# Optimization experiments

Measured on AMD Instinct MI355X. Metric: run time of the kernel, lower is better.

Reference implementation:

```python
import jax, jax.numpy as jnp
import numpy as np

S, B, H, T = 1024, 32, 1024, 512


def setup_inputs() -> dict:
    key = jax.random.key(0)
    ks = jax.random.split(key, 7)
    scale = 1.0 / np.sqrt(H)
    return {
        "hidden": jax.random.normal(ks[0], (S, B, H), dtype=jnp.float32),
        "x": jax.random.normal(ks[1], (B, T, H), dtype=jnp.float32),
        "problem_q": jax.random.normal(ks[2], (B, H), dtype=jnp.float32),
        "K_w": jax.random.normal(ks[3], (H, H), dtype=jnp.float32) * scale,
        "K_b": jax.random.normal(ks[4], (H,), dtype=jnp.float32) * scale,
        "V_w": jax.random.normal(ks[5], (H, H), dtype=jnp.float32) * scale,
        "V_b": jax.random.normal(ks[6], (H,), dtype=jnp.float32) * scale,
    }


def reference(hidden, x, problem_q, K_w, K_b, V_w, V_b):
    # hidden: [S, B, H] -> hidden2: [B, S, H]
    hidden2 = jnp.transpose(hidden, (1, 0, 2))
    # Linear projections (torch Linear: y = x @ W.T + b)
    k = jnp.einsum("bsh,kh->bsk", hidden2, K_w) + K_b  # [B, S, H]
    v = jnp.einsum("bsh,kh->bsk", hidden2, V_w) + V_b  # [B, S, H]
    # scores[b,t,s] = x[b,t] . k[b,s]  (QK^T per batch)
    scores = jnp.einsum("bth,bsh->bts", x, k)
    attn = jax.nn.softmax(scores, axis=-1)  # softmax over encoder positions S
    out = jax.nn.sigmoid(jnp.einsum("bts,bsh->bth", attn, v))  # [B, T, H]
    return out
```

## Files before the change

### kernel.cpp

```cpp
#include <hip/hip_runtime.h>

typedef unsigned short u16;
typedef __attribute__((ext_vector_type(8))) short short8;
typedef __attribute__((ext_vector_type(8))) _Float16 half8;
typedef __attribute__((ext_vector_type(4))) float f32x4;
typedef __attribute__((ext_vector_type(4))) u16 u16x4;
typedef __attribute__((ext_vector_type(4))) unsigned int u32x4;

#define DEVINL static __device__ __forceinline__

DEVINL u16 f2bf(float f) {
  unsigned u = __builtin_bit_cast(unsigned, f);
  u += 0x7fffu + ((u >> 16) & 1u);
  return (u16)(u >> 16);
}
DEVINL float bf2f(u16 h) {
  return __builtin_bit_cast(float, ((unsigned)h) << 16);
}
DEVINL u16 f2h(float f) { return __builtin_bit_cast(u16, (_Float16)f); }
DEVINL float h2f(u16 h) { return (float)__builtin_bit_cast(_Float16, h); }

DEVINL void gload16(const void* g, void* l) {
  __builtin_amdgcn_global_load_lds(
      (const __attribute__((address_space(1))) void*)g,
      (__attribute__((address_space(3))) void*)l, 16, 0, 0);
}

#define BAR() asm volatile("s_barrier" ::: "memory")
#define WAIT_VM0() asm volatile("s_waitcnt vmcnt(0)" ::: "memory")
#define WAIT_LGKM0() asm volatile("s_waitcnt lgkmcnt(0)" ::: "memory")


__global__ __launch_bounds__(256) void cvt_hidden2_k(const float* __restrict__ hid,
                                                     u16* __restrict__ hf,
                                                     u16* __restrict__ hT) {
  __shared__ u16 tl[64][72];
  const int s0 = blockIdx.x * 64;
  const int h0 = blockIdx.y * 64;
  const int b = blockIdx.z;
  const int t = threadIdx.x;
  const int r = t >> 4;
  const int c4 = (t & 15) * 4;
#pragma unroll
  for (int it = 0; it < 4; ++it) {
    const int s = it * 16 + r;
    const f32x4 v = *(const f32x4*)(hid + ((size_t)(s0 + s) * 32 + b) * 1024 + h0 + c4);
    u16x4 of;
#pragma unroll
    for (int j = 0; j < 4; ++j) {
      of[j] = f2h(v[j]);
      tl[s][c4 + j] = f2bf(v[j]);
    }
    *(u16x4*)(hf + ((size_t)b * 1024 + s0 + s) * 1024 + h0 + c4) = of;
  }
  __syncthreads();
  const int h = t >> 2;
  const int sq = (t & 3) * 16;
  u16 tmp[16] __attribute__((aligned(16)));
#pragma unroll
  for (int i = 0; i < 16; ++i) tmp[i] = tl[sq + i][h];
  u16* dst = hT + ((size_t)b * 1024 + h0 + h) * 1024 + s0 + sq;
  *(u32x4*)(dst) = *(const u32x4*)&tmp[0];
  *(u32x4*)(dst + 8) = *(const u32x4*)&tmp[8];
}

__global__ __launch_bounds__(256) void cvt_split_k(const float* __restrict__ in,
                                                   u16* __restrict__ hi_o,
                                                   u16* __restrict__ lo_o, long n4) {
  long i = (long)blockIdx.x * 256 + threadIdx.x;
  const long stride = (long)gridDim.x * 256;
  for (; i < n4; i += stride) {
    const f32x4 v = ((const f32x4*)in)[i];
    u16x4 oh, ol;
#pragma unroll
    for (int j = 0; j < 4; ++j) {
      const u16 hi = f2bf(v[j]);
      oh[j] = hi;
      ol[j] = f2bf(v[j] - bf2f(hi));
    }
    ((u16x4*)hi_o)[i] = oh;
    ((u16x4*)lo_o)[i] = ol;
  }
}

__global__ __launch_bounds__(256) void cvt_f32_bf16_k(const float* __restrict__ in,
                                                      u16* __restrict__ out, long n4) {
  long i = (long)blockIdx.x * 256 + threadIdx.x;
  const long stride = (long)gridDim.x * 256;
  for (; i < n4; i += stride) {
    const f32x4 v = ((const f32x4*)in)[i];
    u16x4 o;
#pragma unroll
    for (int j = 0; j < 4; ++j) o[j] = f2bf(v[j]);
    ((u16x4*)out)[i] = o;
  }
}

__global__ __launch_bounds__(256) void cvt_w_split_t_k(const float* __restrict__ in,
                                                       u16* __restrict__ hi_o,
                                                       u16* __restrict__ lo_o) {
  __shared__ float tile[64][65];
  const int bh = blockIdx.x * 64;
  const int bj = blockIdx.y * 64;
  const int t = threadIdx.x;
  const int r = t >> 4;
  const int c4 = (t & 15) * 4;
#pragma unroll
  for (int it = 0; it < 4; ++it) {
    const int row = it * 16 + r;
    const f32x4 v = *(const f32x4*)(in + (size_t)(bj + row) * 1024 + bh + c4);
#pragma unroll
    for (int j = 0; j < 4; ++j) tile[c4 + j][row] = v[j];
  }
  __syncthreads();
#pragma unroll
  for (int it = 0; it < 4; ++it) {
    const int hrow = it * 16 + r;
    u16x4 oh, ol;
#pragma unroll
    for (int j = 0; j < 4; ++j) {
      const float f = tile[hrow][c4 + j];
      const u16 hv = f2bf(f);
      oh[j] = hv;
      ol[j] = f2bf(f - bf2f(hv));
    }
    *(u16x4*)(hi_o + (size_t)(bh + hrow) * 1024 + bj + c4) = oh;
    *(u16x4*)(lo_o + (size_t)(bh + hrow) * 1024 + bj + c4) = ol;
  }
}

__global__ __launch_bounds__(512) void gemm3_8ph_k(
    const u16* __restrict__ Ah, const u16* __restrict__ Al,
    const u16* __restrict__ Bh, const u16* __restrict__ Bl,
    u16* __restrict__ Chi, u16* __restrict__ Clo) {
  __shared__ u16 lds[2][2][256 * 64];
  const int bid = blockIdx.x;
  const int swz = (bid & 7) * 32 + (bid >> 3);
  const int m0 = (swz >> 2) * 256;
  const int n0 = (swz & 3) * 256;
  const int tid = threadIdx.x;
  const int lane = tid & 63, wid = tid >> 6;
  const int wr = wid >> 2, wc = wid & 3;
  const int fr = lane & 15, fk = lane >> 4;

  f32x4 acc[8][4] = {};

#define STAGE3(pb, q, gph, gpl, rb, kt)                                        \
  {                                                                            \
    _Pragma("unroll") for (int j = 0; j < 4; ++j) {                            \
      const int slot = j * 512 + tid;                                          \
      const int r = slot >> 3;                                                 \
      const int g = (slot & 7) ^ (r & 7);                                      \
      const u16* src = (g < 4) ? (gph) : (gpl);                                \
      gload16(src + (size_t)((rb) + r) * 1024 + (kt) * 32 + (g & 3) * 8,       \
              &lds[pb][q][(j * 512 + wid * 64) * 8]);                          \
    }                                                                          \
  }

  STAGE3(0, 0, Ah, Al, m0, 0);
  STAGE3(0, 1, Bh, Bl, n0, 0);

  for (int t = 0; t < 32; ++t) {
    const int p = t & 1;
    WAIT_VM0();
    BAR();
    short8 bh[4], bl[4];
#pragma unroll
    for (int ph = 0; ph < 4; ++ph) {
      short8 ah[2], al[2];
#pragma unroll
      for (int i = 0; i < 2; ++i) {
        const int r = wr * 128 + (ph * 2 + i) * 16 + fr;
        const int ch = fk ^ (r & 7);
        ah[i] = *(const short8*)&lds[p][0][r * 64 + ch * 8];
        al[i] = *(const short8*)&lds[p][0][r * 64 + (ch ^ 4) * 8];
      }
      if (ph == 0) {
#pragma unroll
        for (int nf = 0; nf < 4; ++nf) {
          const int rn = wc * 64 + nf * 16 + fr;
          const int cn = fk ^ (rn & 7);
          bh[nf] = *(const short8*)&lds[p][1][rn * 64 + cn * 8];
          bl[nf] = *(const short8*)&lds[p][1][rn * 64 + (cn ^ 4) * 8];
        }
        if (t < 31) STAGE3(p ^ 1, 0, Ah, Al, m0, t + 1);
      }
      if (ph == 1 && t < 31) STAGE3(p ^ 1, 1, Bh, Bl, n0, t + 1);
      BAR();
      WAIT_LGKM0();
      __builtin_amdgcn_sched_barrier(0);
      __builtin_amdgcn_s_setprio(1);
#pragma unroll
      for (int i = 0; i < 2; ++i)
#pragma unroll
        for (int nf = 0; nf < 4; ++nf) {
          acc[ph * 2 + i][nf] =
              __builtin_amdgcn_mfma_f32_16x16x32_bf16(ah[i], bh[nf], acc[ph * 2 + i][nf], 0, 0, 0);
          acc[ph * 2 + i][nf] =
              __builtin_amdgcn_mfma_f32_16x16x32_bf16(ah[i], bl[nf], acc[ph * 2 + i][nf], 0, 0, 0);
          acc[ph * 2 + i][nf] =
              __builtin_amdgcn_mfma_f32_16x16x32_bf16(al[i], bh[nf], acc[ph * 2 + i][nf], 0, 0, 0);
        }
      __builtin_amdgcn_s_setprio(0);
      BAR();
    }
  }
#undef STAGE3

  const int cb = n0 + wc * 64 + fr;
  const int rb = m0 + wr * 128 + fk * 4;
#pragma unroll
  for (int mf = 0; mf < 8; ++mf)
#pragma unroll
    for (int nf = 0; nf < 4; ++nf) {
      const int col = cb + nf * 16;
#pragma unroll
      for (int j = 0; j < 4; ++j) {
        const int row = rb + mf * 16 + j;
        const float kv = acc[mf][nf][j];
        const u16 hi = f2h(kv);
        Chi[(size_t)row * 1024 + col] = hi;
        Clo[(size_t)row * 1024 + col] = f2h(kv - h2f(hi));
      }
    }
}

__global__ __launch_bounds__(512) void gemm2_8ph_k(
    const u16* __restrict__ Qh_, const u16* __restrict__ Ql_,
    const u16* __restrict__ Hf_, float* __restrict__ S) {
  __shared__ u16 lA[2][256 * 64];
  __shared__ u16 lB[2][256 * 32];
  const int bid = blockIdx.x;
  const int swz = (bid & 7) * 32 + (bid >> 3);
  const int z = swz >> 3;
  const int m0 = ((swz >> 2) & 1) * 256;
  const int n0 = (swz & 3) * 256;
  const u16* Qh = Qh_ + (size_t)z * 512 * 1024;
  const u16* Ql = Ql_ + (size_t)z * 512 * 1024;
  const u16* Hf = Hf_ + (size_t)z * 1024 * 1024;
  float* Cf = S + (size_t)z * 512 * 1024;
  const int tid = threadIdx.x;
  const int lane = tid & 63, wid = tid >> 6;
  const int wr = wid >> 2, wc = wid & 3;
  const int fr = lane & 15, fk = lane >> 4;

  f32x4 acc[8][4] = {};

#define STAGEA(pb, kt)                                                         \
  {                                                                            \
    _Pragma("unroll") for (int j = 0; j < 4; ++j) {                            \
      const int slot = j * 512 + tid;                                          \
      const int r = slot >> 3;                                                 \
      const int g = (slot & 7) ^ (r & 7);                                      \
      const u16* src = (g < 4) ? Qh : Ql;                                      \
      gload16(src + (size_t)(m0 + r) * 1024 + (kt) * 32 + (g & 3) * 8,         \
              &lA[pb][(j * 512 + wid * 64) * 8]);                              \
    }                                                                          \
  }
#define STAGEB(pb, kt)                                                         \
  {                                                                            \
    _Pragma("unroll") for (int j = 0; j < 2; ++j) {                            \
      const int slot = j * 512 + tid;                                          \
      const int r = slot >> 2;                                                 \
      const int g = (slot & 3) ^ ((r >> 1) & 3);                               \
      gload16(Hf + (size_t)(n0 + r) * 1024 + (kt) * 32 + g * 8,                \
              &lB[pb][(j * 512 + wid * 64) * 8]);                              \
    }                                                                          \
  }

  STAGEA(0, 0);
  STAGEB(0, 0);

  for (int t = 0; t < 32; ++t) {
    const int p = t & 1;
    WAIT_VM0();
    BAR();
    half8 bf[4];
#pragma unroll
    for (int ph = 0; ph < 4; ++ph) {
      half8 ah[2], al[2];
#pragma unroll
      for (int i = 0; i < 2; ++i) {
        const int r = wr * 128 + (ph * 2 + i) * 16 + fr;
        const int ch = fk ^ (r & 7);
        ah[i] = *(const half8*)&lA[p][r * 64 + ch * 8];
        al[i] = *(const half8*)&lA[p][r * 64 + (ch ^ 4) * 8];
      }
      if (ph == 0) {
#pragma unroll
        for (int nf = 0; nf < 4; ++nf) {
          const int rn = wc * 64 + nf * 16 + fr;
          const int cn = fk ^ ((rn >> 1) & 3);
          bf[nf] = *(const half8*)&lB[p][rn * 32 + cn * 8];
        }
        if (t < 31) STAGEA(p ^ 1, t + 1);
      }
      if (ph == 1 && t < 31) STAGEB(p ^ 1, t + 1);
      BAR();
      WAIT_LGKM0();
      __builtin_amdgcn_sched_barrier(0);
      __builtin_amdgcn_s_setprio(1);
#pragma unroll
      for (int i = 0; i < 2; ++i)
#pragma unroll
        for (int nf = 0; nf < 4; ++nf) {
          acc[ph * 2 + i][nf] =
              __builtin_amdgcn_mfma_f32_16x16x32_f16(ah[i], bf[nf], acc[ph * 2 + i][nf], 0, 0, 0);
          acc[ph * 2 + i][nf] =
              __builtin_amdgcn_mfma_f32_16x16x32_f16(al[i], bf[nf], acc[ph * 2 + i][nf], 0, 0, 0);
        }
      __builtin_amdgcn_s_setprio(0);
      BAR();
    }
  }
#undef STAGEA
#undef STAGEB

  const int cb = n0 + wc * 64 + fr;
  const int rb = m0 + wr * 128 + fk * 4;
#pragma unroll
  for (int mf = 0; mf < 8; ++mf)
#pragma unroll
    for (int nf = 0; nf < 4; ++nf) {
      const int col = cb + nf * 16;
#pragma unroll
      for (int j = 0; j < 4; ++j) {
        const int row = rb + mf * 16 + j;
        Cf[(size_t)row * 1024 + col] = acc[mf][nf][j];
      }
    }
}

template <int CM>
__global__ __launch_bounds__(512) void gemm1_8ph_k(
    const u16* __restrict__ A_, const u16* __restrict__ Bt_,
    const float* __restrict__ bias, void* __restrict__ Cout) {
  __shared__ u16 lds[2][2][256 * 64];
  const int bid = blockIdx.x;
  const int swz = (bid & 7) * 32 + (bid >> 3);
  int m0, n0;
  const u16 *A, *Bt;
  float* Cf = nullptr;
  u16* Cb = nullptr;
  if (CM == 0) {
    const int z = swz >> 3;
    m0 = ((swz >> 2) & 1) * 256;
    n0 = (swz & 3) * 256;
    A = A_ + (size_t)z * 512 * 1024;
    Bt = Bt_ + (size_t)z * 1024 * 1024;
    Cb = (u16*)Cout + (size_t)z * 512 * 1024;
  } else {
    m0 = (swz >> 2) * 256;
    n0 = (swz & 3) * 256;
    A = A_; Bt = Bt_;
    Cf = (float*)Cout;
  }
  const int tid = threadIdx.x;
  const int lane = tid & 63, wid = tid >> 6;
  const int wr = wid >> 2, wc = wid & 3;
  const int fr = lane & 15, fk = lane >> 4;

  f32x4 acc[8][4] = {};

#define STAGE1(pb, q, gp, rb, kt)                                              \
  {                                                                            \
    _Pragma("unroll") for (int j = 0; j < 4; ++j) {                            \
      const int slot = j * 512 + tid;                                          \
      const int r = slot >> 3;                                                 \
      const int g = (slot & 7) ^ (r & 7);                                      \
      gload16((gp) + (size_t)((rb) + r) * 1024 + (kt) * 64 + g * 8,            \
              &lds[pb][q][(j * 512 + wid * 64) * 8]);                          \
    }                                                                          \
  }

  STAGE1(0, 0, A, m0, 0);
  STAGE1(0, 1, Bt, n0, 0);

  for (int t = 0; t < 16; ++t) {
    const int p = t & 1;
    WAIT_VM0();
    BAR();
    short8 bfr[4][2];
#pragma unroll
    for (int ph = 0; ph < 4; ++ph) {
      short8 a[2][2];
#pragma unroll
      for (int i = 0; i < 2; ++i) {
        const int r = wr * 128 + (ph * 2 + i) * 16 + fr;
#pragma unroll
        for (int ks = 0; ks < 2; ++ks) {
          const int g = (ks * 4 + fk) ^ (r & 7);
          a[i][ks] = *(const short8*)&lds[p][0][r * 64 + g * 8];
        }
      }
      if (ph == 0) {
#pragma unroll
        for (int nf = 0; nf < 4; ++nf) {
          const int rn = wc * 64 + nf * 16 + fr;
#pragma unroll
          for (int ks = 0; ks < 2; ++ks) {
            const int g = (ks * 4 + fk) ^ (rn & 7);
            bfr[nf][ks] = *(const short8*)&lds[p][1][rn * 64 + g * 8];
          }
        }
        if (t < 15) {
          STAGE1(p ^ 1, 0, A, m0, t + 1);
          STAGE1(p ^ 1, 1, Bt, n0, t + 1);
        }
      }
      BAR();
      WAIT_LGKM0();
      __builtin_amdgcn_sched_barrier(0);
      __builtin_amdgcn_s_setprio(1);
#pragma unroll
      for (int i = 0; i < 2; ++i)
#pragma unroll
        for (int nf = 0; nf < 4; ++nf) {
          acc[ph * 2 + i][nf] = __builtin_amdgcn_mfma_f32_16x16x32_bf16(
              a[i][0], bfr[nf][0], acc[ph * 2 + i][nf], 0, 0, 0);
          acc[ph * 2 + i][nf] = __builtin_amdgcn_mfma_f32_16x16x32_bf16(
              a[i][1], bfr[nf][1], acc[ph * 2 + i][nf], 0, 0, 0);
        }
      __builtin_amdgcn_s_setprio(0);
      BAR();
    }
  }
#undef STAGE1

  const int cb = n0 + wc * 64 + fr;
  const int rb = m0 + wr * 128 + fk * 4;
  if (CM == 0) {
#pragma unroll
    for (int mf = 0; mf < 8; ++mf)
#pragma unroll
      for (int nf = 0; nf < 4; ++nf) {
        const int col = cb + nf * 16;
#pragma unroll
        for (int j = 0; j < 4; ++j) {
          const int row = rb + mf * 16 + j;
          Cb[(size_t)row * 1024 + col] = f2bf(acc[mf][nf][j]);
        }
      }
  } else {
#pragma unroll
    for (int mf = 0; mf < 8; ++mf)
#pragma unroll
      for (int nf = 0; nf < 4; ++nf) {
        const int col = cb + nf * 16;
        const float bv = bias[col];
#pragma unroll
        for (int j = 0; j < 4; ++j) {
          const int row = rb + mf * 16 + j;
          const float xv = acc[mf][nf][j] + bv;
          Cf[(size_t)row * 1024 + col] = 1.0f / (1.0f + __expf(-xv));
        }
      }
  }
}

__global__ __launch_bounds__(256) void softmax_k(const float* __restrict__ S,
                                                 u16* __restrict__ Attn) {
  const float* rp = S + (size_t)blockIdx.x * 1024;
  const int tid = threadIdx.x;
  const int lane = tid & 63, wid = tid >> 6;
  const f32x4 v = ((const f32x4*)rp)[tid];
  float mx = fmaxf(fmaxf(v[0], v[1]), fmaxf(v[2], v[3]));
#pragma unroll
  for (int off = 32; off; off >>= 1) mx = fmaxf(mx, __shfl_xor(mx, off));
  __shared__ float red[4];
  __shared__ float red2[4];
  if (lane == 0) red[wid] = mx;
  __syncthreads();
  mx = fmaxf(fmaxf(red[0], red[1]), fmaxf(red[2], red[3]));
  const float e0 = __expf(v[0] - mx), e1 = __expf(v[1] - mx);
  const float e2 = __expf(v[2] - mx), e3 = __expf(v[3] - mx);
  float s = (e0 + e1) + (e2 + e3);
#pragma unroll
  for (int off = 32; off; off >>= 1) s += __shfl_xor(s, off);
  if (lane == 0) red2[wid] = s;
  __syncthreads();
  const float inv = 1.0f / (red2[0] + red2[1] + red2[2] + red2[3]);
  u16x4 o;
  o[0] = f2bf(e0 * inv); o[1] = f2bf(e1 * inv); o[2] = f2bf(e2 * inv); o[3] = f2bf(e3 * inv);
  ((u16x4*)(Attn + (size_t)blockIdx.x * 1024))[tid] = o;
}

extern "C" void kernel_launch(void* const* d_in, const int* in_sizes, int n_in,
                              void* d_out, int out_size, void* d_ws, size_t ws_size,
                              hipStream_t stream) {
  const float* hidden = (const float*)d_in[0];
  const float* x = (const float*)d_in[1];
  const float* K_w = (const float*)d_in[3];
  const float* V_w = (const float*)d_in[5];
  const float* V_b = (const float*)d_in[6];

  char* ws = (char*)d_ws;
  u16* hf16 = (u16*)(ws);
  u16* hT = (u16*)(ws + 67108864);
  u16* qhi = (u16*)(ws + 134217728);
  u16* qlo = (u16*)(ws + 167772160);
  float* scoresF = (float*)(ws + 201326592);
  u16* attn = hf16;
  u16* ctx = qhi;
  u16* kwt_h = (u16*)(ws + 268435456);
  u16* kwt_l = kwt_h + 1024 * 1024;
  u16* vw = kwt_h + 2 * 1024 * 1024;
  u16* xhi = (u16*)d_out;
  u16* xlo = xhi + 32L * 512 * 1024;
  float* out = (float*)d_out;

  cvt_hidden2_k<<<dim3(16, 16, 32), 256, 0, stream>>>(hidden, hf16, hT);
  cvt_split_k<<<2048, 256, 0, stream>>>(x, xhi, xlo, 32L * 512 * 1024 / 4);
  cvt_w_split_t_k<<<dim3(16, 16), 256, 0, stream>>>(K_w, kwt_h, kwt_l);
  cvt_f32_bf16_k<<<1024, 256, 0, stream>>>(V_w, vw, 1024L * 1024 / 4);
  gemm3_8ph_k<<<256, 512, 0, stream>>>(xhi, xlo, kwt_h, kwt_l, qhi, qlo);
  gemm2_8ph_k<<<256, 512, 0, stream>>>(qhi, qlo, hf16, scoresF);
  softmax_k<<<16384, 256, 0, stream>>>(scoresF, attn);
  gemm1_8ph_k<0><<<256, 512, 0, stream>>>(attn, hT, nullptr, ctx);
  gemm1_8ph_k<1><<<256, 512, 0, stream>>>(ctx, vw, V_b, out);
}
```

Measured before the change: 349.4 us.

## Replace 3-pass bf16 split Q projection with 2-pass fp16 split GEMM

The x·K_w^T projection moves from a three-MFMA bf16 hi/lo split (hi*hi, hi*lo, lo*hi) to an fp16 split of x only, with K_w converted to a single fp16 matrix. The gemm2 kernel is templated so one code path serves both this projection and the scores GEMM, cutting MFMA work and the bytes loaded for the weight operand. The transpose tile in cvt_hidden2_k is also XOR-swizzled to reduce LDS bank conflicts. The trade is accuracy: K_w now carries only fp16 precision, and fp16 has less range than bf16.

```diff
diff --git a/kernel.cpp b/kernel.cpp
--- a/kernel.cpp
+++ b/kernel.cpp
@@ -46,10 +46,11 @@
     const int s = it * 16 + r;
     const f32x4 v = *(const f32x4*)(hid + ((size_t)(s0 + s) * 32 + b) * 1024 + h0 + c4);
     u16x4 of;
+    const int cs = c4 ^ (it << 2);
 #pragma unroll
     for (int j = 0; j < 4; ++j) {
       of[j] = f2h(v[j]);
-      tl[s][c4 + j] = f2bf(v[j]);
+      tl[s][cs + j] = f2bf(v[j]);
     }
     *(u16x4*)(hf + ((size_t)b * 1024 + s0 + s) * 1024 + h0 + c4) = of;
   }
@@ -58,15 +59,16 @@
   const int sq = (t & 3) * 16;
   u16 tmp[16] __attribute__((aligned(16)));
 #pragma unroll
-  for (int i = 0; i < 16; ++i) tmp[i] = tl[sq + i][h];
+  for (int i = 0; i < 16; ++i)
+    tmp[i] = tl[sq + i][h ^ ((((sq + i) >> 4) & 3) << 2)];
   u16* dst = hT + ((size_t)b * 1024 + h0 + h) * 1024 + s0 + sq;
   *(u32x4*)(dst) = *(const u32x4*)&tmp[0];
   *(u32x4*)(dst + 8) = *(const u32x4*)&tmp[8];
 }
 
-__global__ __launch_bounds__(256) void cvt_split_k(const float* __restrict__ in,
-                                                   u16* __restrict__ hi_o,
-                                                   u16* __restrict__ lo_o, long n4) {
+__global__ __launch_bounds__(256) void cvt_split_h_k(const float* __restrict__ in,
+                                                     u16* __restrict__ hi_o,
+                                                     u16* __restrict__ lo_o, long n4) {
   long i = (long)blockIdx.x * 256 + threadIdx.x;
   const long stride = (long)gridDim.x * 256;
   for (; i < n4; i += stride) {
@@ -74,9 +76,9 @@
     u16x4 oh, ol;
 #pragma unroll
     for (int j = 0; j < 4; ++j) {
-      const u16 hi = f2bf(v[j]);
+      const u16 hi = f2h(v[j]);
       oh[j] = hi;
-      ol[j] = f2bf(v[j] - bf2f(hi));
+      ol[j] = f2h(v[j] - h2f(hi));
     }
     ((u16x4*)hi_o)[i] = oh;
     ((u16x4*)lo_o)[i] = ol;
@@ -96,9 +98,8 @@
   }
 }
 
-__global__ __launch_bounds__(256) void cvt_w_split_t_k(const float* __restrict__ in,
-                                                       u16* __restrict__ hi_o,
-                                                       u16* __restrict__ lo_o) {
+__global__ __launch_bounds__(256) void cvt_w_t_h_k(const float* __restrict__ in,
+                                                   u16* __restrict__ out) {
   __shared__ float tile[64][65];
   const int bh = blockIdx.x * 64;
   const int bj = blockIdx.y * 64;
@@ -116,129 +117,39 @@
 #pragma unroll
   for (int it = 0; it < 4; ++it) {
     const int hrow = it * 16 + r;
-    u16x4 oh, ol;
-#pragma unroll
-    for (int j = 0; j < 4; ++j) {
-      const float f = tile[hrow][c4 + j];
-      const u16 hv = f2bf(f);
-      oh[j] = hv;
-      ol[j] = f2bf(f - bf2f(hv));
-    }
-    *(u16x4*)(hi_o + (size_t)(bh + hrow) * 1024 + bj + c4) = oh;
-    *(u16x4*)(lo_o + (size_t)(bh + hrow) * 1024 + bj + c4) = ol;
-  }
-}
-
-__global__ __launch_bounds__(512) void gemm3_8ph_k(
-    const u16* __restrict__ Ah, const u16* __restrict__ Al,
-    const u16* __restrict__ Bh, const u16* __restrict__ Bl,
-    u16* __restrict__ Chi, u16* __restrict__ Clo) {
-  __shared__ u16 lds[2][2][256 * 64];
-  const int bid = blockIdx.x;
-  const int swz = (bid & 7) * 32 + (bid >> 3);
-  const int m0 = (swz >> 2) * 256;
-  const int n0 = (swz & 3) * 256;
-  const int tid = threadIdx.x;
-  const int lane = tid & 63, wid = tid >> 6;
-  const int wr = wid >> 2, wc = wid & 3;
-  const int fr = lane & 15, fk = lane >> 4;
-
-  f32x4 acc[8][4] = {};
-
-#define STAGE3(pb, q, gph, gpl, rb, kt)                                        \
-  {                                                                            \
-    _Pragma("unroll") for (int j = 0; j < 4; ++j) {                            \
-      const int slot = j * 512 + tid;                                          \
-      const int r = slot >> 3;                                                 \
-      const int g = (slot & 7) ^ (r & 7);                                      \
-      const u16* src = (g < 4) ? (gph) : (gpl);                                \
-      gload16(src + (size_t)((rb) + r) * 1024 + (kt) * 32 + (g & 3) * 8,       \
-              &lds[pb][q][(j * 512 + wid * 64) * 8]);                          \
-    }                                                                          \
-  }
-
-  STAGE3(0, 0, Ah, Al, m0, 0);
-  STAGE3(0, 1, Bh, Bl, n0, 0);
-
-  for (int t = 0; t < 32; ++t) {
-    const int p = t & 1;
-    WAIT_VM0();
-    BAR();
-    short8 bh[4], bl[4];
-#pragma unroll
-    for (int ph = 0; ph < 4; ++ph) {
-      short8 ah[2], al[2];
-#pragma unroll
-      for (int i = 0; i < 2; ++i) {
-        const int r = wr * 128 + (ph * 2 + i) * 16 + fr;
-        const int ch = fk ^ (r & 7);
-        ah[i] = *(const short8*)&lds[p][0][r * 64 + ch * 8];
-        al[i] = *(const short8*)&lds[p][0][r * 64 + (ch ^ 4) * 8];
-      }
-      if (ph == 0) {
-#pragma unroll
-        for (int nf = 0; nf < 4; ++nf) {
-          const int rn = wc * 64 + nf * 16 + fr;
-          const int cn = fk ^ (rn & 7);
-          bh[nf] = *(const short8*)&lds[p][1][rn * 64 + cn * 8];
-          bl[nf] = *(const short8*)&lds[p][1][rn * 64 + (cn ^ 4) * 8];
-        }
-        if (t < 31) STAGE3(p ^ 1, 0, Ah, Al, m0, t + 1);
-      }
-      if (ph == 1 && t < 31) STAGE3(p ^ 1, 1, Bh, Bl, n0, t + 1);
-      BAR();
-      WAIT_LGKM0();
-      __builtin_amdgcn_sched_barrier(0);
-      __builtin_amdgcn_s_setprio(1);
-#pragma unroll
-      for (int i = 0; i < 2; ++i)
-#pragma unroll
-        for (int nf = 0; nf < 4; ++nf) {
-          acc[ph * 2 + i][nf] =
-              __builtin_amdgcn_mfma_f32_16x16x32_bf16(ah[i], bh[nf], acc[ph * 2 + i][nf], 0, 0, 0);
-          acc[ph * 2 + i][nf] =
-              __builtin_amdgcn_mfma_f32_16x16x32_bf16(ah[i], bl[nf], acc[ph * 2 + i][nf], 0, 0, 0);
-          acc[ph * 2 + i][nf] =
-              __builtin_amdgcn_mfma_f32_16x16x32_bf16(al[i], bh[nf], acc[ph * 2 + i][nf], 0, 0, 0);
-        }
-      __builtin_amdgcn_s_setprio(0);
-      BAR();
-    }
-  }
-#undef STAGE3
-
-  const int cb = n0 + wc * 64 + fr;
-  const int rb = m0 + wr * 128 + fk * 4;
-#pragma unroll
-  for (int mf = 0; mf < 8; ++mf)
-#pragma unroll
-    for (int nf = 0; nf < 4; ++nf) {
-      const int col = cb + nf * 16;
-#pragma unroll
-      for (int j = 0; j < 4; ++j) {
-        const int row = rb + mf * 16 + j;
-        const float kv = acc[mf][nf][j];
-        const u16 hi = f2h(kv);
-        Chi[(size_t)row * 1024 + col] = hi;
-        Clo[(size_t)row * 1024 + col] = f2h(kv - h2f(hi));
-      }
-    }
-}
-
+    u16x4 of;
+#pragma unroll
+    for (int j = 0; j < 4; ++j) of[j] = f2h(tile[hrow][c4 + j]);
+    *(u16x4*)(out + (size_t)(bh + hrow) * 1024 + bj + c4) = of;
+  }
+}
+
+template <int CM>
 __global__ __launch_bounds__(512) void gemm2_8ph_k(
-    const u16* __restrict__ Qh_, const u16* __restrict__ Ql_,
-    const u16* __restrict__ Hf_, float* __restrict__ S) {
+    const u16* __restrict__ Ah_, const u16* __restrict__ Al_,
+    const u16* __restrict__ B_, void* __restrict__ C0, void* __restrict__ C1) {
   __shared__ u16 lA[2][256 * 64];
   __shared__ u16 lB[2][256 * 32];
   const int bid = blockIdx.x;
   const int swz = (bid & 7) * 32 + (bid >> 3);
-  const int z = swz >> 3;
-  const int m0 = ((swz >> 2) & 1) * 256;
-  const int n0 = (swz & 3) * 256;
-  const u16* Qh = Qh_ + (size_t)z * 512 * 1024;
-  const u16* Ql = Ql_ + (size_t)z * 512 * 1024;
-  const u16* Hf = Hf_ + (size_t)z * 1024 * 1024;
-  float* Cf = S + (size_t)z * 512 * 1024;
+  int m0, n0;
+  const u16 *Ah, *Al, *Bm;
+  float* Cf = nullptr;
+  u16 *Chi = nullptr, *Clo = nullptr;
+  if (CM == 0) {
+    m0 = (swz >> 2) * 256;
+    n0 = (swz & 3) * 256;
+    Ah = Ah_; Al = Al_; Bm = B_;
+    Chi = (u16*)C0; Clo = (u16*)C1;
+  } else {
+    const int z = swz >> 3;
+    m0 = ((swz >> 2) & 1) * 256;
+    n0 = (swz & 3) * 256;
+    Ah = Ah_ + (size_t)z * 512 * 1024;
+    Al = Al_ + (size_t)z * 512 * 1024;
+    Bm = B_ + (size_t)z * 1024 * 1024;
+    Cf = (float*)C0 + (size_t)z * 512 * 1024;
+  }
   const int tid = threadIdx.x;
   const int lane = tid & 63, wid = tid >> 6;
   const int wr = wid >> 2, wc = wid & 3;
@@ -252,7 +163,7 @@
       const int slot = j * 512 + tid;                                          \
       const int r = slot >> 3;                                                 \
       const int g = (slot & 7) ^ (r & 7);                                      \
-      const u16* src = (g < 4) ? Qh : Ql;                                      \
+      const u16* src = (g < 4) ? Ah : Al;                                      \
       gload16(src + (size_t)(m0 + r) * 1024 + (kt) * 32 + (g & 3) * 8,         \
               &lA[pb][(j * 512 + wid * 64) * 8]);                              \
     }                                                                          \
@@ -263,7 +174,7 @@
       const int slot = j * 512 + tid;                                          \
       const int r = slot >> 2;                                                 \
       const int g = (slot & 3) ^ ((r >> 1) & 3);                               \
-      gload16(Hf + (size_t)(n0 + r) * 1024 + (kt) * 32 + g * 8,                \
+      gload16(Bm + (size_t)(n0 + r) * 1024 + (kt) * 32 + g * 8,                \
               &lB[pb][(j * 512 + wid * 64) * 8]);                              \
     }                                                                          \
   }
@@ -318,17 +229,34 @@
 
   const int cb = n0 + wc * 64 + fr;
   const int rb = m0 + wr * 128 + fk * 4;
-#pragma unroll
-  for (int mf = 0; mf < 8; ++mf)
-#pragma unroll
-    for (int nf = 0; nf < 4; ++nf) {
-      const int col = cb + nf * 16;
-#pragma unroll
-      for (int j = 0; j < 4; ++j) {
-        const int row = rb + mf * 16 + j;
-        Cf[(size_t)row * 1024 + col] = acc[mf][nf][j];
-      }
-    }
+  if (CM == 0) {
+#pragma unroll
+    for (int mf = 0; mf < 8; ++mf)
+#pragma unroll
+      for (int nf = 0; nf < 4; ++nf) {
+        const int col = cb + nf * 16;
+#pragma unroll
+        for (int j = 0; j < 4; ++j) {
+          const int row = rb + mf * 16 + j;
+          const float kv = acc[mf][nf][j];
+          const u16 hi = f2h(kv);
+          Chi[(size_t)row * 1024 + col] = hi;
+          Clo[(size_t)row * 1024 + col] = f2h(kv - h2f(hi));
+        }
+      }
+  } else {
+#pragma unroll
+    for (int mf = 0; mf < 8; ++mf)
+#pragma unroll
+      for (int nf = 0; nf < 4; ++nf) {
+        const int col = cb + nf * 16;
+#pragma unroll
+        for (int j = 0; j < 4; ++j) {
+          const int row = rb + mf * 16 + j;
+          Cf[(size_t)row * 1024 + col] = acc[mf][nf][j];
+        }
+      }
+  }
 }
 
 template <int CM>
@@ -502,19 +430,18 @@
   float* scoresF = (float*)(ws + 201326592);
   u16* attn = hf16;
   u16* ctx = qhi;
-  u16* kwt_h = (u16*)(ws + 268435456);
-  u16* kwt_l = kwt_h + 1024 * 1024;
-  u16* vw = kwt_h + 2 * 1024 * 1024;
+  u16* kwT = (u16*)(ws + 268435456);
+  u16* vw = kwT + 1024 * 1024;
   u16* xhi = (u16*)d_out;
   u16* xlo = xhi + 32L * 512 * 1024;
   float* out = (float*)d_out;
 
   cvt_hidden2_k<<<dim3(16, 16, 32), 256, 0, stream>>>(hidden, hf16, hT);
-  cvt_split_k<<<2048, 256, 0, stream>>>(x, xhi, xlo, 32L * 512 * 1024 / 4);
-  cvt_w_split_t_k<<<dim3(16, 16), 256, 0, stream>>>(K_w, kwt_h, kwt_l);
+  cvt_split_h_k<<<2048, 256, 0, stream>>>(x, xhi, xlo, 32L * 512 * 1024 / 4);
+  cvt_w_t_h_k<<<dim3(16, 16), 256, 0, stream>>>(K_w, kwT);
   cvt_f32_bf16_k<<<1024, 256, 0, stream>>>(V_w, vw, 1024L * 1024 / 4);
-  gemm3_8ph_k<<<256, 512, 0, stream>>>(xhi, xlo, kwt_h, kwt_l, qhi, qlo);
-  gemm2_8ph_k<<<256, 512, 0, stream>>>(qhi, qlo, hf16, scoresF);
+  gemm2_8ph_k<0><<<256, 512, 0, stream>>>(xhi, xlo, kwT, qhi, qlo);
+  gemm2_8ph_k<1><<<256, 512, 0, stream>>>(qhi, qlo, hf16, scoresF, nullptr);
   softmax_k<<<16384, 256, 0, stream>>>(scoresF, attn);
   gemm1_8ph_k<0><<<256, 512, 0, stream>>>(attn, hT, nullptr, ctx);
   gemm1_8ph_k<1><<<256, 512, 0, stream>>>(ctx, vw, V_b, out);
```

Result: faster. 338.2 us (-3.2%).
